# Kernel optimization log

Measured on AMD Instinct MI355X. Metric: run time of the kernel, lower is better.

The kernel has to match this reference:

```python
import jax, jax.numpy as jnp
import numpy as np

D = 1024
H = 16
HD = D // H
FF = 4 * D
LN_EPS = 1e-5


def _layernorm(x, w, b):
    mu = jnp.mean(x, axis=-1, keepdims=True)
    var = jnp.mean(jnp.square(x - mu), axis=-1, keepdims=True)
    return (x - mu) * jax.lax.rsqrt(var + LN_EPS) * w + b


def setup_inputs() -> dict:
    key = jax.random.key(0)
    ks = jax.random.split(key, 12)
    s = 0.02
    return {
        "x": jax.random.normal(ks[0], (8, 1024, D), jnp.float32),
        "c": jax.random.normal(ks[1], (8, D), jnp.float32),
        "ln1_w": jnp.ones((D,), jnp.float32),
        "ln1_b": jnp.zeros((D,), jnp.float32),
        "ln2_w": jnp.ones((D,), jnp.float32),
        "ln2_b": jnp.zeros((D,), jnp.float32),
        "ada_w": jax.random.normal(ks[2], (D, 6 * D), jnp.float32) * s,
        "ada_b": jnp.zeros((6 * D,), jnp.float32),
        "qkv_w": jax.random.normal(ks[3], (D, 3 * D), jnp.float32) * s,
        "qkv_b": jnp.zeros((3 * D,), jnp.float32),
        "proj_w": jax.random.normal(ks[4], (D, D), jnp.float32) * s,
        "proj_b": jnp.zeros((D,), jnp.float32),
        "fc1_w": jax.random.normal(ks[5], (D, FF), jnp.float32) * s,
        "fc1_b": jnp.zeros((FF,), jnp.float32),
        "fc2_w": jax.random.normal(ks[6], (FF, D), jnp.float32) * s,
        "fc2_b": jnp.zeros((D,), jnp.float32),
    }


def reference(x, c, ln1_w, ln1_b, ln2_w, ln2_b, ada_w, ada_b,
              qkv_w, qkv_b, proj_w, proj_b, fc1_w, fc1_b, fc2_w, fc2_b):
    B, L, _ = x.shape
    # adaLN modulation: SiLU(c) @ W -> 6 chunks of (B, D)
    ssg = jax.nn.silu(c) @ ada_w + ada_b
    msa_shift, msa_scale, msa_gate, mlp_shift, mlp_scale, mlp_gate = jnp.split(ssg, 6, axis=-1)

    def modulate(h, shift, scale):
        return h * (1.0 + scale[:, None, :]) + shift[:, None, :]

    # ---- attention branch ----
    h = modulate(_layernorm(x, ln1_w, ln1_b), msa_shift, msa_scale)
    qkv = h @ qkv_w + qkv_b                      # (B, L, 3D)
    q, k, v = jnp.split(qkv, 3, axis=-1)
    q = q.reshape(B, L, H, HD).transpose(0, 2, 1, 3)   # (B, H, L, HD)
    k = k.reshape(B, L, H, HD).transpose(0, 2, 1, 3)
    v = v.reshape(B, L, H, HD).transpose(0, 2, 1, 3)
    scores = jnp.einsum("bhqd,bhkd->bhqk", q, k) / jnp.sqrt(jnp.float32(HD))
    attn = jax.nn.softmax(scores, axis=-1)
    a = jnp.einsum("bhqk,bhkd->bhqd", attn, v)   # (B, H, L, HD)
    a = a.transpose(0, 2, 1, 3).reshape(B, L, D)
    a = a @ proj_w + proj_b
    x = x + msa_gate[:, None, :] * a

    # ---- MLP branch ----
    h = modulate(_layernorm(x, ln2_w, ln2_b), mlp_shift, mlp_scale)
    h = jax.nn.gelu(h @ fc1_w + fc1_b, approximate=True)
    h = h @ fc2_w + fc2_b
    x = x + mlp_gate[:, None, :] * h
    return x
```

## Files before the change

kernel.cpp:

```cpp
#include <hip/hip_runtime.h>
#include <math.h>

#define DMODEL 1024
#define SIXD   6144
#define NHEAD  16
#define HEADD  64
#define LSEQ   1024
#define NBATCH 8
#define MROWS  8192

typedef unsigned short ushort_t;
typedef __attribute__((ext_vector_type(8))) short bf16x8;
typedef __attribute__((ext_vector_type(4))) float f32x4;

__device__ __forceinline__ unsigned short f2bf(float f) {
  unsigned int u = __float_as_uint(f);
  u += 0x7fff + ((u >> 16) & 1);
  return (unsigned short)(u >> 16);
}

__device__ __forceinline__ void gload_lds16(const void* g, void* l) {
  __builtin_amdgcn_global_load_lds(
      (const __attribute__((address_space(1))) unsigned int*)g,
      (__attribute__((address_space(3))) unsigned int*)l, 16, 0, 0);
}

__global__ void tcast_kernel(const float* __restrict__ W, ushort_t* __restrict__ WT,
                             int K, int N) {
  __shared__ float tile[32][33];
  int tx = threadIdx.x & 31, ty = threadIdx.x >> 5;
  int n0 = blockIdx.x * 32, k0 = blockIdx.y * 32;
#pragma unroll
  for (int r = 0; r < 4; ++r)
    tile[ty + 8*r][tx] = W[(size_t)(k0 + ty + 8*r) * N + n0 + tx];
  __syncthreads();
#pragma unroll
  for (int r = 0; r < 4; ++r)
    WT[(size_t)(n0 + ty + 8*r) * K + k0 + tx] = f2bf(tile[tx][ty + 8*r]);
}

__global__ void ada_kernel(const float* __restrict__ c, const float* __restrict__ ada_w,
                           const float* __restrict__ ada_b, float* __restrict__ ssg) {
  __shared__ float s[DMODEL];
  int b = blockIdx.y;
  int j = blockIdx.x * 256 + threadIdx.x;
  for (int i = threadIdx.x; i < DMODEL; i += 256) {
    float v = c[b * DMODEL + i];
    s[i] = v / (1.0f + __expf(-v));
  }
  __syncthreads();
  float acc = ada_b[j];
#pragma unroll 8
  for (int k = 0; k < DMODEL; ++k)
    acc = fmaf(s[k], ada_w[(size_t)k * SIXD + j], acc);
  ssg[b * SIXD + j] = acc;
}

__global__ __launch_bounds__(256) void ln_mod_kernel(
    const float* __restrict__ xin, const float* __restrict__ lw,
    const float* __restrict__ lb, const float* __restrict__ ssg,
    int shift_off, int scale_off, ushort_t* __restrict__ outB) {
  int row = blockIdx.x;
  int b = row >> 10;
  int tid = threadIdx.x;
  float4 v = ((const float4*)xin)[(size_t)row * 256 + tid];
  float sum = v.x + v.y + v.z + v.w;
  float sq  = v.x*v.x + v.y*v.y + v.z*v.z + v.w*v.w;
#pragma unroll
  for (int m = 32; m; m >>= 1) { sum += __shfl_xor(sum, m); sq += __shfl_xor(sq, m); }
  __shared__ float rbuf[8];
  int w = tid >> 6, lane = tid & 63;
  if (lane == 0) { rbuf[w] = sum; rbuf[4 + w] = sq; }
  __syncthreads();
  sum = rbuf[0] + rbuf[1] + rbuf[2] + rbuf[3];
  sq  = rbuf[4] + rbuf[5] + rbuf[6] + rbuf[7];
  float mu  = sum * (1.0f / 1024.0f);
  float var = sq * (1.0f / 1024.0f) - mu * mu;
  float rs  = rsqrtf(var + 1e-5f);
  const float* sg = ssg + b * SIXD;
  float vv[4] = {v.x, v.y, v.z, v.w};
  ushort4 pk;
  unsigned short* pks = (unsigned short*)&pk;
#pragma unroll
  for (int j = 0; j < 4; ++j) {
    int d = tid * 4 + j;
    float h = (vv[j] - mu) * rs * lw[d] + lb[d];
    h = h * (1.0f + sg[scale_off + d]) + sg[shift_off + d];
    pks[j] = f2bf(h);
  }
  ((ushort4*)outB)[(size_t)row * 256 + tid] = pk;
}

template <int EPI>
__global__ __launch_bounds__(256, 2) void gemm_kernel(
    const ushort_t* __restrict__ A, const ushort_t* __restrict__ BT,
    const float* __restrict__ bias, const float* __restrict__ ssg,
    const float* resid, float* outF, ushort_t* __restrict__ outB,
    int N, int K, int gate_off) {
  __shared__ __align__(16) char As[16384];
  __shared__ __align__(16) char Bs[16384];
  int tid = threadIdx.x, lane = tid & 63, w = tid >> 6;
  int l15 = lane & 15, g = lane >> 4;
  int m0 = blockIdx.y * 128, n0 = blockIdx.x * 128;
  int wrow = (w >> 1) * 64, wcol = (w & 1) * 64;
  f32x4 zero = {0.f, 0.f, 0.f, 0.f};
  f32x4 acc[4][4];
#pragma unroll
  for (int i = 0; i < 4; ++i)
#pragma unroll
    for (int j = 0; j < 4; ++j) acc[i][j] = zero;

  for (int k0 = 0; k0 < K; k0 += 64) {
#pragma unroll
    for (int p = 0; p < 4; ++p) {
      int flat = p * 4096 + w * 1024 + lane * 16;
      int row = flat >> 7;
      int colb = (flat & 127) ^ ((row & 7) << 4);
      gload_lds16((const char*)A  + ((size_t)(m0 + row) * K + k0) * 2 + colb,
                  As + p * 4096 + w * 1024);
      gload_lds16((const char*)BT + ((size_t)(n0 + row) * K + k0) * 2 + colb,
                  Bs + p * 4096 + w * 1024);
    }
    __syncthreads();
#pragma unroll
    for (int kk = 0; kk < 2; ++kk) {
      bf16x8 af[4], bfr[4];
#pragma unroll
      for (int i = 0; i < 4; ++i) {
        int ar = wrow + i * 16 + l15;
        af[i]  = *(const bf16x8*)(As + ar * 128 + ((kk * 64 + g * 16) ^ ((ar & 7) << 4)));
        int br = wcol + i * 16 + l15;
        bfr[i] = *(const bf16x8*)(Bs + br * 128 + ((kk * 64 + g * 16) ^ ((br & 7) << 4)));
      }
#pragma unroll
      for (int i = 0; i < 4; ++i)
#pragma unroll
        for (int j = 0; j < 4; ++j)
          acc[i][j] = __builtin_amdgcn_mfma_f32_16x16x32_bf16(af[i], bfr[j], acc[i][j], 0, 0, 0);
    }
    __syncthreads();
  }
#pragma unroll
  for (int i = 0; i < 4; ++i)
#pragma unroll
    for (int j = 0; j < 4; ++j)
#pragma unroll
      for (int r = 0; r < 4; ++r) {
        int grow = m0 + wrow + i * 16 + g * 4 + r;
        int gcol = n0 + wcol + j * 16 + l15;
        float v = acc[i][j][r] + bias[gcol];
        if (EPI == 0) {
          outB[(size_t)grow * N + gcol] = f2bf(v);
        } else if (EPI == 1 || EPI == 3) {
          int bb = grow >> 10;
          float gate = ssg[bb * SIXD + gate_off + gcol];
          size_t idx = (size_t)grow * N + gcol;
          outF[idx] = resid[idx] + gate * v;
        } else {
          float u = v;
          float t = 0.7978845608028654f * (u + 0.044715f * u * u * u);
          float e = __expf(2.0f * t);
          float th = 1.0f - 2.0f / (e + 1.0f);
          outB[(size_t)grow * N + gcol] = f2bf(0.5f * u * (1.0f + th));
        }
      }
}

__global__ __launch_bounds__(256, 2) void attn_kernel(
    const ushort_t* __restrict__ qkv,
    ushort_t* __restrict__ aout) {
  __shared__ __align__(16) char SM[33024];
  float* alphab = (float*)(SM + 32768);
  int tid = threadIdx.x, lane = tid & 63, w = tid >> 6;
  int l15 = lane & 15, g = lane >> 4;
  int qt = blockIdx.x, bh = blockIdx.y;
  int b = bh >> 4, h = bh & 15;

  bf16x8 aq[2];
  {
    int qrow = qt * 64 + w * 16 + l15;
    const short* qp = (const short*)qkv + (size_t)(b * LSEQ + qrow) * 3072 + h * 64 + g * 8;
    aq[0] = *(const bf16x8*)qp;
    aq[1] = *(const bf16x8*)(qp + 32);
  }

  const char* ksrc[2];
#pragma unroll
  for (int p = 0; p < 2; ++p) {
    int flat = p * 4096 + w * 1024 + lane * 16;
    int row = flat >> 7;
    int colb = (flat & 127) ^ ((row & 7) << 4);
    ksrc[p] = (const char*)qkv + ((size_t)(b * LSEQ + row) * 3072 + 1024 + h * 64) * 2 + colb;
  }
  const short* vsrc[2];
  int vkv[2], vdc[2];
#pragma unroll
  for (int i = 0; i < 2; ++i) {
    int flat = tid + 256 * i;
    vkv[i] = flat >> 3;
    vdc[i] = flat & 7;
    vsrc[i] = (const short*)qkv + (size_t)(b * LSEQ + vkv[i]) * 3072 + 2048 + h * 64 + vdc[i] * 8;
  }

  f32x4 zero = {0.f, 0.f, 0.f, 0.f};
  f32x4 o[4] = {zero, zero, zero, zero};
  float mrow = -INFINITY;
  float lrow = 0.f;
  const float sc = 0.18033688f;

#pragma unroll
  for (int p = 0; p < 2; ++p) gload_lds16(ksrc[p], SM + p * 4096 + w * 1024);
#pragma unroll
  for (int i = 0; i < 2; ++i) {
    bf16x8 vv = *(const bf16x8*)vsrc[i];
    char* vb = SM + 16384;
#pragma unroll
    for (int j = 0; j < 8; ++j) {
      int d = vdc[i] * 8 + j;
      *(short*)(vb + d * 128 + ((vkv[i] * 2) ^ ((d & 7) << 4))) = vv[j];
    }
  }
  __syncthreads();

  for (int t = 0; t < 16; ++t) {
    int cur = t & 1;
    bf16x8 vn[2];
    if (t < 15) {
      size_t koff = (size_t)(t + 1) * (64 * 3072 * 2);
#pragma unroll
      for (int p = 0; p < 2; ++p)
        gload_lds16(ksrc[p] + koff, SM + (cur ^ 1) * 8192 + p * 4096 + w * 1024);
#pragma unroll
      for (int i = 0; i < 2; ++i)
        vn[i] = *(const bf16x8*)(vsrc[i] + (size_t)(t + 1) * (64 * 3072));
    }
    f32x4 s4[4] = {zero, zero, zero, zero};
#pragma unroll
    for (int c = 0; c < 4; ++c)
#pragma unroll
      for (int ks = 0; ks < 2; ++ks) {
        int key = c * 16 + l15;
        bf16x8 ak = *(const bf16x8*)(SM + cur * 8192 + key * 128 +
                                     ((ks * 64 + g * 16) ^ ((key & 7) << 4)));
        s4[c] = __builtin_amdgcn_mfma_f32_16x16x32_bf16(ak, aq[ks], s4[c], 0, 0, 0);
      }
    float z[16], mx = -INFINITY;
#pragma unroll
    for (int c = 0; c < 4; ++c)
#pragma unroll
      for (int r = 0; r < 4; ++r) {
        float t2 = s4[c][r] * sc;
        z[c * 4 + r] = t2;
        mx = fmaxf(mx, t2);
      }
    mx = fmaxf(mx, __shfl_xor(mx, 16));
    mx = fmaxf(mx, __shfl_xor(mx, 32));
    bool need = __any(mx > mrow);
    if (need) {
      float mnew = fmaxf(mrow, mx);
      float alpha = exp2f(mrow - mnew);
      mrow = mnew;
      if (lane < 16) alphab[w * 16 + lane] = alpha;
      lrow *= alpha;
    }
    float p16[16], sump = 0.f;
#pragma unroll
    for (int i = 0; i < 16; ++i) {
      float p = exp2f(z[i] - mrow);
      p16[i] = p;
      sump += p;
    }
    sump += __shfl_xor(sump, 16);
    sump += __shfl_xor(sump, 32);
    lrow += sump;
    if (need) {
      f32x4 av = *(const f32x4*)&alphab[w * 16 + g * 4];
#pragma unroll
      for (int nb = 0; nb < 4; ++nb)
#pragma unroll
        for (int r = 0; r < 4; ++r) o[nb][r] *= av[r];
    }
    unsigned pk[8];
#pragma unroll
    for (int c = 0; c < 4; ++c)
#pragma unroll
      for (int m = 0; m < 2; ++m)
        asm("v_cvt_pk_bf16_f32 %0, %1, %2"
            : "=v"(pk[c * 2 + m]) : "v"(p16[c * 4 + 2 * m]), "v"(p16[c * 4 + 2 * m + 1]));
    unsigned pa[2][4];
    int gl = (g & 1) * 2;
#pragma unroll
    for (int kb = 0; kb < 2; ++kb)
#pragma unroll
      for (int wv = 0; wv < 4; ++wv) {
        int srcl = l15 + (gl + (wv >> 1)) * 16;
        unsigned vA = (unsigned)__shfl((int)pk[kb * 4 + (wv & 1)], srcl);
        unsigned vB = (unsigned)__shfl((int)pk[kb * 4 + 2 + (wv & 1)], srcl);
        pa[kb][wv] = (g >> 1) ? vB : vA;
      }
    if (t < 15) {
      char* vb = SM + 16384 + (cur ^ 1) * 8192;
#pragma unroll
      for (int i = 0; i < 2; ++i)
#pragma unroll
        for (int j = 0; j < 8; ++j) {
          int d = vdc[i] * 8 + j;
          *(short*)(vb + d * 128 + ((vkv[i] * 2) ^ ((d & 7) << 4))) = vn[i][j];
        }
    }
    union PU { unsigned u[4]; bf16x8 v; };
    PU pu0, pu1;
#pragma unroll
    for (int i = 0; i < 4; ++i) { pu0.u[i] = pa[0][i]; pu1.u[i] = pa[1][i]; }
#pragma unroll
    for (int kb = 0; kb < 2; ++kb)
#pragma unroll
      for (int nb = 0; nb < 4; ++nb) {
        int d = nb * 16 + l15;
        bf16x8 bv = *(const bf16x8*)(SM + 16384 + cur * 8192 + d * 128 +
                                     ((kb * 64 + g * 16) ^ ((d & 7) << 4)));
        o[nb] = __builtin_amdgcn_mfma_f32_16x16x32_bf16(kb ? pu1.v : pu0.v, bv, o[nb], 0, 0, 0);
      }
    __syncthreads();
  }
  if (lane < 16) alphab[w * 16 + lane] = 1.0f / lrow;
  f32x4 rl = *(const f32x4*)&alphab[w * 16 + g * 4];
#pragma unroll
  for (int nb = 0; nb < 4; ++nb)
#pragma unroll
    for (int r = 0; r < 4; ++r) {
      int qrow = qt * 64 + w * 16 + g * 4 + r;
      aout[(size_t)(b * LSEQ + qrow) * 1024 + h * 64 + nb * 16 + l15] =
          f2bf(o[nb][r] * rl[r]);
    }
}

extern "C" void kernel_launch(void* const* d_in, const int* in_sizes, int n_in,
                              void* d_out, int out_size, void* d_ws, size_t ws_size,
                              hipStream_t stream) {
  const float* x      = (const float*)d_in[0];
  const float* c      = (const float*)d_in[1];
  const float* ln1_w  = (const float*)d_in[2];
  const float* ln1_b  = (const float*)d_in[3];
  const float* ln2_w  = (const float*)d_in[4];
  const float* ln2_b  = (const float*)d_in[5];
  const float* ada_w  = (const float*)d_in[6];
  const float* ada_b  = (const float*)d_in[7];
  const float* qkv_w  = (const float*)d_in[8];
  const float* qkv_b  = (const float*)d_in[9];
  const float* proj_w = (const float*)d_in[10];
  const float* proj_b = (const float*)d_in[11];
  const float* fc1_w  = (const float*)d_in[12];
  const float* fc1_b  = (const float*)d_in[13];
  const float* fc2_w  = (const float*)d_in[14];
  const float* fc2_b  = (const float*)d_in[15];
  float* out = (float*)d_out;
  char* ws = (char*)d_ws;

  ushort_t* qkvT  = (ushort_t*)(ws + 0);
  ushort_t* projT = (ushort_t*)(ws + 6291456);
  ushort_t* fc1T  = (ushort_t*)(ws + 8388608);
  ushort_t* fc2T  = (ushort_t*)(ws + 16777216);
  float*    ssg   = (float*)(ws + 25165824);
  ushort_t* hbuf  = (ushort_t*)(ws + 25362432);
  ushort_t* abuf  = hbuf;
  ushort_t* qkvb  = (ushort_t*)(ws + 42139648);
  if (ws_size < (size_t)109248512) return;

  tcast_kernel<<<dim3(96, 32),  256, 0, stream>>>(qkv_w,  qkvT, 1024, 3072);
  tcast_kernel<<<dim3(32, 32),  256, 0, stream>>>(proj_w, projT, 1024, 1024);
  tcast_kernel<<<dim3(128, 32), 256, 0, stream>>>(fc1_w,  fc1T, 1024, 4096);
  tcast_kernel<<<dim3(32, 128), 256, 0, stream>>>(fc2_w,  fc2T, 4096, 1024);
  ada_kernel<<<dim3(24, 8), 256, 0, stream>>>(c, ada_w, ada_b, ssg);

  ln_mod_kernel<<<8192, 256, 0, stream>>>(x, ln1_w, ln1_b, ssg, 0, 1024, hbuf);
  gemm_kernel<0><<<dim3(24, 64), 256, 0, stream>>>(hbuf, qkvT, qkv_b, nullptr,
                                                   nullptr, nullptr, qkvb, 3072, 1024, 0);
  attn_kernel<<<dim3(16, 128), 256, 0, stream>>>(qkvb, abuf);
  gemm_kernel<1><<<dim3(8, 64), 256, 0, stream>>>(abuf, projT, proj_b, ssg,
                                                  x, out, nullptr, 1024, 1024, 2048);
  ln_mod_kernel<<<8192, 256, 0, stream>>>(out, ln2_w, ln2_b, ssg, 3072, 4096, hbuf);
  gemm_kernel<2><<<dim3(32, 64), 256, 0, stream>>>(hbuf, fc1T, fc1_b, nullptr,
                                                   nullptr, nullptr, qkvb, 4096, 1024, 0);
  gemm_kernel<3><<<dim3(8, 64), 256, 0, stream>>>(qkvb, fc2T, fc2_b, ssg,
                                                  out, out, nullptr, 1024, 4096, 5120);
}
```

Measured before the change: 475.8 us.

## Pre-transpose V into a separate buffer and stream it via direct LDS loads

Adds a kernel that transposes the V slice of the QKV output into a per-head [d][key] layout. The attention kernel then loads V tiles with the same global-to-LDS async loads used for K, replacing per-element scattered shared-memory stores done through registers inside the loop. This removes per-iteration register transpose work and LDS bank-unfriendly short stores, at the cost of an extra kernel launch and an extra 16MB read/write pass over V.

After: 443.2 us. 1.07x faster.

```diff
diff --git a/kernel.cpp b/kernel.cpp
--- a/kernel.cpp
+++ b/kernel.cpp
@@ -37,6 +37,34 @@
 #pragma unroll
   for (int r = 0; r < 4; ++r)
     WT[(size_t)(n0 + ty + 8*r) * K + k0 + tx] = f2bf(tile[tx][ty + 8*r]);
+}
+
+__global__ __launch_bounds__(256) void vtrans_kernel(
+    const ushort_t* __restrict__ qkvb, ushort_t* __restrict__ vT) {
+  __shared__ ushort_t tile[128][66];
+  int bh = blockIdx.x;
+  int kt = blockIdx.y;
+  int b = bh >> 4, h = bh & 15;
+  int tid = threadIdx.x;
+#pragma unroll
+  for (int i = 0; i < 4; ++i) {
+    int flat = tid + 256 * i;
+    int r = flat >> 3, c8 = flat & 7;
+    bf16x8 v = *(const bf16x8*)((const short*)qkvb +
+        (size_t)(b * LSEQ + kt * 128 + r) * 3072 + 2048 + h * 64 + c8 * 8);
+#pragma unroll
+    for (int j = 0; j < 8; ++j) tile[r][c8 * 8 + j] = (ushort_t)v[j];
+  }
+  __syncthreads();
+#pragma unroll
+  for (int i = 0; i < 4; ++i) {
+    int d = i * 16 + (tid >> 4);
+    int kc = tid & 15;
+    bf16x8 ov;
+#pragma unroll
+    for (int j = 0; j < 8; ++j) ov[j] = (short)tile[kc * 8 + j][d];
+    *(bf16x8*)((short*)vT + (size_t)(bh * 64 + d) * 1024 + kt * 128 + kc * 8) = ov;
+  }
 }
 
 __global__ void ada_kernel(const float* __restrict__ c, const float* __restrict__ ada_w,
@@ -168,6 +196,7 @@
 
 __global__ __launch_bounds__(256, 2) void attn_kernel(
     const ushort_t* __restrict__ qkv,
+    const ushort_t* __restrict__ vT,
     ushort_t* __restrict__ aout) {
   __shared__ __align__(16) char SM[33024];
   float* alphab = (float*)(SM + 32768);
@@ -185,21 +214,14 @@
   }
 
   const char* ksrc[2];
+  const char* vsrc[2];
 #pragma unroll
   for (int p = 0; p < 2; ++p) {
     int flat = p * 4096 + w * 1024 + lane * 16;
     int row = flat >> 7;
     int colb = (flat & 127) ^ ((row & 7) << 4);
     ksrc[p] = (const char*)qkv + ((size_t)(b * LSEQ + row) * 3072 + 1024 + h * 64) * 2 + colb;
-  }
-  const short* vsrc[2];
-  int vkv[2], vdc[2];
-#pragma unroll
-  for (int i = 0; i < 2; ++i) {
-    int flat = tid + 256 * i;
-    vkv[i] = flat >> 3;
-    vdc[i] = flat & 7;
-    vsrc[i] = (const short*)qkv + (size_t)(b * LSEQ + vkv[i]) * 3072 + 2048 + h * 64 + vdc[i] * 8;
+    vsrc[p] = (const char*)vT + ((size_t)(bh * 64 + row) * 1024) * 2 + colb;
   }
 
   f32x4 zero = {0.f, 0.f, 0.f, 0.f};
@@ -209,30 +231,22 @@
   const float sc = 0.18033688f;
 
 #pragma unroll
-  for (int p = 0; p < 2; ++p) gload_lds16(ksrc[p], SM + p * 4096 + w * 1024);
-#pragma unroll
-  for (int i = 0; i < 2; ++i) {
-    bf16x8 vv = *(const bf16x8*)vsrc[i];
-    char* vb = SM + 16384;
-#pragma unroll
-    for (int j = 0; j < 8; ++j) {
-      int d = vdc[i] * 8 + j;
-      *(short*)(vb + d * 128 + ((vkv[i] * 2) ^ ((d & 7) << 4))) = vv[j];
-    }
+  for (int p = 0; p < 2; ++p) {
+    gload_lds16(ksrc[p], SM + p * 4096 + w * 1024);
+    gload_lds16(vsrc[p], SM + 16384 + p * 4096 + w * 1024);
   }
   __syncthreads();
 
   for (int t = 0; t < 16; ++t) {
     int cur = t & 1;
-    bf16x8 vn[2];
     if (t < 15) {
       size_t koff = (size_t)(t + 1) * (64 * 3072 * 2);
-#pragma unroll
-      for (int p = 0; p < 2; ++p)
+      size_t voff = (size_t)(t + 1) * 128;
+#pragma unroll
+      for (int p = 0; p < 2; ++p) {
         gload_lds16(ksrc[p] + koff, SM + (cur ^ 1) * 8192 + p * 4096 + w * 1024);
-#pragma unroll
-      for (int i = 0; i < 2; ++i)
-        vn[i] = *(const bf16x8*)(vsrc[i] + (size_t)(t + 1) * (64 * 3072));
+        gload_lds16(vsrc[p] + voff, SM + 16384 + (cur ^ 1) * 8192 + p * 4096 + w * 1024);
+      }
     }
     f32x4 s4[4] = {zero, zero, zero, zero};
 #pragma unroll
@@ -298,16 +312,6 @@
         unsigned vB = (unsigned)__shfl((int)pk[kb * 4 + 2 + (wv & 1)], srcl);
         pa[kb][wv] = (g >> 1) ? vB : vA;
       }
-    if (t < 15) {
-      char* vb = SM + 16384 + (cur ^ 1) * 8192;
-#pragma unroll
-      for (int i = 0; i < 2; ++i)
-#pragma unroll
-        for (int j = 0; j < 8; ++j) {
-          int d = vdc[i] * 8 + j;
-          *(short*)(vb + d * 128 + ((vkv[i] * 2) ^ ((d & 7) << 4))) = vn[i][j];
-        }
-    }
     union PU { unsigned u[4]; bf16x8 v; };
     PU pu0, pu1;
 #pragma unroll
@@ -365,6 +369,7 @@
   ushort_t* hbuf  = (ushort_t*)(ws + 25362432);
   ushort_t* abuf  = hbuf;
   ushort_t* qkvb  = (ushort_t*)(ws + 42139648);
+  ushort_t* vTb   = (ushort_t*)(ws + 92471296);
   if (ws_size < (size_t)109248512) return;
 
   tcast_kernel<<<dim3(96, 32),  256, 0, stream>>>(qkv_w,  qkvT, 1024, 3072);
@@ -376,7 +381,8 @@
   ln_mod_kernel<<<8192, 256, 0, stream>>>(x, ln1_w, ln1_b, ssg, 0, 1024, hbuf);
   gemm_kernel<0><<<dim3(24, 64), 256, 0, stream>>>(hbuf, qkvT, qkv_b, nullptr,
                                                    nullptr, nullptr, qkvb, 3072, 1024, 0);
-  attn_kernel<<<dim3(16, 128), 256, 0, stream>>>(qkvb, abuf);
+  vtrans_kernel<<<dim3(128, 8), 256, 0, stream>>>(qkvb, vTb);
+  attn_kernel<<<dim3(16, 128), 256, 0, stream>>>(qkvb, vTb, abuf);
   gemm_kernel<1><<<dim3(8, 64), 256, 0, stream>>>(abuf, projT, proj_b, ssg,
                                                   x, out, nullptr, 1024, 1024, 2048);
   ln_mod_kernel<<<8192, 256, 0, stream>>>(out, ln2_w, ln2_b, ssg, 3072, 4096, hbuf);
```
